# Performance work log

Hardware: AMD Instinct MI355X
Metric: run time of the kernel (lower is better)

The kernel has to match this reference:

```python
import jax, jax.numpy as jnp
import numpy as np

B, T, D = 32, 1024, 768
H = 768          # GRU hidden size
INNER = 512      # fc output size
NOUT = 39        # out_proj outputs (13 classes x 3 ACCDOA coords)


def setup_inputs() -> dict:
    key = jax.random.key(0)
    ks = jax.random.split(key, 16)
    s_in = 1.0 / np.sqrt(H)
    inp = {
        "features": jax.random.normal(ks[0], (B, T, D), jnp.float32),
        "padding_mask": jnp.zeros((B, T), jnp.bool_),
        # GRU layer 0 (input D -> H), PyTorch gate order [r, z, n]
        "w_ih0": jax.random.uniform(ks[1], (3 * H, D), jnp.float32, -s_in, s_in),
        "w_hh0": jax.random.uniform(ks[2], (3 * H, H), jnp.float32, -s_in, s_in),
        "b_ih0": jax.random.uniform(ks[3], (3 * H,), jnp.float32, -s_in, s_in),
        "b_hh0": jax.random.uniform(ks[4], (3 * H,), jnp.float32, -s_in, s_in),
        # GRU layer 1 (H -> H)
        "w_ih1": jax.random.uniform(ks[5], (3 * H, H), jnp.float32, -s_in, s_in),
        "w_hh1": jax.random.uniform(ks[6], (3 * H, H), jnp.float32, -s_in, s_in),
        "b_ih1": jax.random.uniform(ks[7], (3 * H,), jnp.float32, -s_in, s_in),
        "b_hh1": jax.random.uniform(ks[8], (3 * H,), jnp.float32, -s_in, s_in),
        # fc: hidden -> inner, then SELU
        "fc_w": jax.random.uniform(ks[9], (INNER, H), jnp.float32, -s_in, s_in),
        "fc_b": jax.random.uniform(ks[10], (INNER,), jnp.float32, -s_in, s_in),
        # out_proj: inner -> num_outs, then tanh
        "out_w": jax.random.uniform(ks[11], (NOUT, INNER), jnp.float32, -1.0 / np.sqrt(INNER), 1.0 / np.sqrt(INNER)),
        "out_b": jax.random.uniform(ks[12], (NOUT,), jnp.float32, -1.0 / np.sqrt(INNER), 1.0 / np.sqrt(INNER)),
    }
    return inp


def _gru_layer(x, w_ih, w_hh, b_ih, b_hh):
    # x: [B, T, Din] -> [B, T, H]; PyTorch GRU math, gate order r,z,n
    b, t, _ = x.shape
    h = w_hh.shape[1]
    # precompute input projections for all timesteps in one big GEMM
    x_proj = jnp.einsum('btd,gd->btg', x, w_ih) + b_ih  # [B, T, 3H]

    def step(h_prev, xp):
        gi_r, gi_z, gi_n = jnp.split(xp, 3, axis=-1)
        gh = h_prev @ w_hh.T + b_hh
        gh_r, gh_z, gh_n = jnp.split(gh, 3, axis=-1)
        r = jax.nn.sigmoid(gi_r + gh_r)
        z = jax.nn.sigmoid(gi_z + gh_z)
        n = jnp.tanh(gi_n + r * gh_n)
        h_new = (1.0 - z) * n + z * h_prev
        return h_new, h_new

    h0 = jnp.zeros((b, h), x.dtype)
    _, ys = jax.lax.scan(step, h0, jnp.swapaxes(x_proj, 0, 1))  # ys: [T, B, H]
    return jnp.swapaxes(ys, 0, 1)


def reference(features, padding_mask, w_ih0, w_hh0, b_ih0, b_hh0,
              w_ih1, w_hh1, b_ih1, b_hh1, fc_w, fc_b, out_w, out_b):
    # dropout_input p=0.0 -> identity (eval); padding_mask unused by forward math
    x = _gru_layer(features, w_ih0, w_hh0, b_ih0, b_hh0)
    x = _gru_layer(x, w_ih1, w_hh1, b_ih1, b_hh1)
    x = jax.nn.selu(x @ fc_w.T + fc_b)          # fc + activation_fn='selu'
    x = jnp.tanh(x @ out_w.T + out_b)           # out_proj + out_activation 'tanh'
    return x
```

## Files before the change

kernel.cpp:

```cpp
#include <hip/hip_runtime.h>
#include <cstdint>

#define GB_M 128
#define GB_N 64
#define GB_K 16

__global__ __launch_bounds__(256) void gemm_bt_f32(
    const float* __restrict__ A, const float* __restrict__ B,
    const float* __restrict__ bias, float* __restrict__ C,
    int Mc, int N, int K, int tc_shift, int Tfull, int t0, int act)
{
  __shared__ float As[GB_K][GB_M + 4];
  __shared__ float Bs[GB_K][GB_N + 4];
  const int tid = threadIdx.x;
  const int m0 = blockIdx.y * GB_M;
  const int n0 = blockIdx.x * GB_N;
  const int tx = tid & 15;
  const int ty = tid >> 4;

  const int tcmask = (1 << tc_shift) - 1;
  int arow[2];
#pragma unroll
  for (int i = 0; i < 2; i++) {
    int f = tid + i * 256;
    int row = f >> 2;
    int rc = m0 + row;
    arow[i] = (rc >> tc_shift) * Tfull + t0 + (rc & tcmask);
  }
  const int akq = tid & 3;
  const int brow = tid >> 2;
  const int bn = n0 + brow;

  float acc[8][4];
#pragma unroll
  for (int i = 0; i < 8; i++)
#pragma unroll
    for (int j = 0; j < 4; j++) acc[i][j] = 0.f;

  for (int k0 = 0; k0 < K; k0 += GB_K) {
#pragma unroll
    for (int i = 0; i < 2; i++) {
      int f = tid + i * 256;
      int row = f >> 2;
      float4 v = *(const float4*)(A + (size_t)arow[i] * K + k0 + akq * 4);
      As[akq * 4 + 0][row] = v.x; As[akq * 4 + 1][row] = v.y;
      As[akq * 4 + 2][row] = v.z; As[akq * 4 + 3][row] = v.w;
    }
    {
      float4 v = make_float4(0.f, 0.f, 0.f, 0.f);
      if (bn < N) v = *(const float4*)(B + (size_t)bn * K + k0 + akq * 4);
      Bs[akq * 4 + 0][brow] = v.x; Bs[akq * 4 + 1][brow] = v.y;
      Bs[akq * 4 + 2][brow] = v.z; Bs[akq * 4 + 3][brow] = v.w;
    }
    __syncthreads();
#pragma unroll
    for (int k = 0; k < GB_K; k++) {
      float4 a0 = *(const float4*)&As[k][ty * 8];
      float4 a1 = *(const float4*)&As[k][ty * 8 + 4];
      float4 b0 = *(const float4*)&Bs[k][tx * 4];
      float av[8] = {a0.x, a0.y, a0.z, a0.w, a1.x, a1.y, a1.z, a1.w};
      float bv[4] = {b0.x, b0.y, b0.z, b0.w};
#pragma unroll
      for (int i = 0; i < 8; i++)
#pragma unroll
        for (int j = 0; j < 4; j++) acc[i][j] += av[i] * bv[j];
    }
    __syncthreads();
  }

#pragma unroll
  for (int j = 0; j < 4; j++) {
    int n = n0 + tx * 4 + j;
    if (n >= N) continue;
    float bz = bias[n];
#pragma unroll
    for (int i = 0; i < 8; i++) {
      int m = m0 + ty * 8 + i;
      float x = acc[i][j] + bz;
      if (act == 1) {
        x = 1.0507009873554805f * (x > 0.f ? x : 1.6732632423543772f * (__expf(x) - 1.f));
      } else if (act == 2) {
        x = tanhf(x);
      }
      C[(size_t)m * N + n] = x;
    }
  }
}

#define RT 384
#define RNWG 256

__device__ __forceinline__ void pollge(const unsigned* fp, unsigned want) {
  while (__hip_atomic_load(fp, __ATOMIC_RELAXED, __HIP_MEMORY_SCOPE_AGENT) < want)
    __builtin_amdgcn_s_sleep(1);
}

__global__ __launch_bounds__(RT, 1) void gru_rec(
    const float* __restrict__ gi, const float* __restrict__ w_hh,
    const float* __restrict__ b_hh, float* __restrict__ hb,
    unsigned* __restrict__ flags, float* __restrict__ seq,
    int t0, int Tc)
{
  __shared__ float Wl[36][776];
  __shared__ float hs[8][776];
  const int wg = blockIdx.x;
  const int jg = wg & 63;
  const int sd = wg >> 6;
  const int j0 = jg * 12;
  const int tid = threadIdx.x;
  const int p  = tid >> 6;
  const int ks = tid & 63;

  unsigned* flagX_my = flags + (((0 * 4 + sd) * 64) + jg) * 16;
  unsigned* flagY_my = flags + (((1 * 4 + sd) * 64) + jg) * 16;

  for (int f = tid; f < 36 * 192; f += RT) {
    int row = f / 192;
    int kq = f - row * 192;
    int gate = row / 12;
    int jl = row - gate * 12;
    float4 v = *(const float4*)(w_hh + (size_t)(gate * 768 + j0 + jl) * 768 + kq * 4);
    *(float4*)&Wl[row][kq * 4] = v;
  }

  const int j2l = (ks >> 2) & 1;
  const int cl  = ks & 3;
  const int j_out  = j0 + 2 * p + j2l;
  const int bX_out = 8 * sd + cl;
  const int bY_out = 8 * sd + 4 + cl;
  const float bhr = b_hh[j_out];
  const float bhz = b_hh[768 + j_out];
  const float bhn = b_hh[1536 + j_out];

  const float* wb[3][2];
#pragma unroll
  for (int g = 0; g < 3; g++)
#pragma unroll
    for (int j2 = 0; j2 < 2; j2++)
      wb[g][j2] = &Wl[g * 12 + 2 * p + j2][0];

  const int sbi = tid / 96;
  const int sk  = tid - sbi * 96;
  const int jgA = (sk * 8) / 12;
  const int jgB = (sk * 8 + 7) / 12;
  const unsigned* fXA = flags + ((0 * 4 + sd) * 64 + jgA) * 16;
  const unsigned* fXB = flags + ((0 * 4 + sd) * 64 + jgB) * 16;
  const unsigned* fYA = flags + ((1 * 4 + sd) * 64 + jgA) * 16;
  const unsigned* fYB = flags + ((1 * 4 + sd) * 64 + jgB) * 16;

  const bool hi4 = (ks & 4) != 0;
  const bool hi2 = (ks & 2) != 0;
  const bool hi1 = (ks & 1) != 0;

  for (int tt = 0; tt < Tc; tt++) {
    const int t = t0 + tt;

    pollge(fXA, (unsigned)t);
    pollge(fXB, (unsigned)t);
    {
      const unsigned long long* src = (const unsigned long long*)
          (hb + (size_t)(t & 1) * 24576 + (size_t)(8 * sd + sbi) * 768) + sk * 4;
      unsigned long long v[4];
#pragma unroll
      for (int i = 0; i < 4; i++)
        v[i] = __hip_atomic_load(src + i, __ATOMIC_RELAXED, __HIP_MEMORY_SCOPE_AGENT);
      float* dst = &hs[sbi][sk * 8];
      *(float4*)dst = make_float4(
          __uint_as_float((unsigned)v[0]), __uint_as_float((unsigned)(v[0] >> 32)),
          __uint_as_float((unsigned)v[1]), __uint_as_float((unsigned)(v[1] >> 32)));
      *(float4*)(dst + 4) = make_float4(
          __uint_as_float((unsigned)v[2]), __uint_as_float((unsigned)(v[2] >> 32)),
          __uint_as_float((unsigned)v[3]), __uint_as_float((unsigned)(v[3] >> 32)));
    }
    float gXr = 0.f, gXz = 0.f, gXn = 0.f;
    if (ks < 8) {
      const float* gX = gi + ((size_t)bX_out * Tc + tt) * 2304 + j_out;
      gXr = gX[0]; gXz = gX[768]; gXn = gX[1536];
    }
    __syncthreads();
    if (tid == 0)
      __hip_atomic_store(flagY_my, (unsigned)t, __ATOMIC_RELAXED, __HIP_MEMORY_SCOPE_AGENT);

    float r3[3];
    {
      float acc[3][2][4];
#pragma unroll
      for (int g = 0; g < 3; g++)
#pragma unroll
        for (int j2 = 0; j2 < 2; j2++)
#pragma unroll
          for (int c = 0; c < 4; c++) acc[g][j2][c] = 0.f;
#pragma unroll
      for (int kk = 0; kk < 3; kk++) {
        const int off = (kk * 64 + ks) * 4;
        float4 h[4];
#pragma unroll
        for (int c = 0; c < 4; c++) h[c] = *(const float4*)(&hs[c][0] + off);
#pragma unroll
        for (int g = 0; g < 3; g++)
#pragma unroll
          for (int j2 = 0; j2 < 2; j2++) {
            float4 w = *(const float4*)(wb[g][j2] + off);
#pragma unroll
            for (int c = 0; c < 4; c++)
              acc[g][j2][c] += w.x * h[c].x + w.y * h[c].y + w.z * h[c].z + w.w * h[c].w;
          }
      }
      float r12[3][4];
#pragma unroll
      for (int g = 0; g < 3; g++)
#pragma unroll
        for (int c = 0; c < 4; c++) {
          float send = hi4 ? acc[g][0][c] : acc[g][1][c];
          float keep = hi4 ? acc[g][1][c] : acc[g][0][c];
          r12[g][c] = keep + __shfl_xor(send, 4);
        }
      float r6[3][2];
#pragma unroll
      for (int g = 0; g < 3; g++)
#pragma unroll
        for (int c2 = 0; c2 < 2; c2++) {
          float send = hi2 ? r12[g][c2] : r12[g][2 + c2];
          float keep = hi2 ? r12[g][2 + c2] : r12[g][c2];
          r6[g][c2] = keep + __shfl_xor(send, 2);
        }
#pragma unroll
      for (int g = 0; g < 3; g++) {
        float send = hi1 ? r6[g][0] : r6[g][1];
        float keep = hi1 ? r6[g][1] : r6[g][0];
        r3[g] = keep + __shfl_xor(send, 1);
      }
#pragma unroll
      for (int g = 0; g < 3; g++) {
        r3[g] += __shfl_xor(r3[g], 8);
        r3[g] += __shfl_xor(r3[g], 16);
        r3[g] += __shfl_xor(r3[g], 32);
      }
    }
    if (ks < 8) {
      float hp = hs[cl][j_out];
      float r = 1.f / (1.f + __expf(-(gXr + r3[0] + bhr)));
      float z = 1.f / (1.f + __expf(-(gXz + r3[1] + bhz)));
      float n = tanhf(gXn + r * (r3[2] + bhn));
      float hv = (1.f - z) * n + z * hp;
      __hip_atomic_store(hb + (size_t)((t + 1) & 1) * 24576 + (size_t)bX_out * 768 + j_out,
                         hv, __ATOMIC_RELAXED, __HIP_MEMORY_SCOPE_AGENT);
      seq[((size_t)bX_out * 1024 + t) * 768 + j_out] = hv;
    }

    pollge(fYA, (unsigned)t);
    pollge(fYB, (unsigned)t);
    {
      const unsigned long long* src = (const unsigned long long*)
          (hb + (size_t)(t & 1) * 24576 + (size_t)(8 * sd + 4 + sbi) * 768) + sk * 4;
      unsigned long long v[4];
#pragma unroll
      for (int i = 0; i < 4; i++)
        v[i] = __hip_atomic_load(src + i, __ATOMIC_RELAXED, __HIP_MEMORY_SCOPE_AGENT);
      float* dst = &hs[4 + sbi][sk * 8];
      *(float4*)dst = make_float4(
          __uint_as_float((unsigned)v[0]), __uint_as_float((unsigned)(v[0] >> 32)),
          __uint_as_float((unsigned)v[1]), __uint_as_float((unsigned)(v[1] >> 32)));
      *(float4*)(dst + 4) = make_float4(
          __uint_as_float((unsigned)v[2]), __uint_as_float((unsigned)(v[2] >> 32)),
          __uint_as_float((unsigned)v[3]), __uint_as_float((unsigned)(v[3] >> 32)));
    }
    float gYr = 0.f, gYz = 0.f, gYn = 0.f;
    if (ks < 8) {
      const float* gY = gi + ((size_t)bY_out * Tc + tt) * 2304 + j_out;
      gYr = gY[0]; gYz = gY[768]; gYn = gY[1536];
    }
    __syncthreads();
    if (tid == 0)
      __hip_atomic_store(flagX_my, (unsigned)(t + 1), __ATOMIC_RELAXED, __HIP_MEMORY_SCOPE_AGENT);

    {
      float acc[3][2][4];
#pragma unroll
      for (int g = 0; g < 3; g++)
#pragma unroll
        for (int j2 = 0; j2 < 2; j2++)
#pragma unroll
          for (int c = 0; c < 4; c++) acc[g][j2][c] = 0.f;
#pragma unroll
      for (int kk = 0; kk < 3; kk++) {
        const int off = (kk * 64 + ks) * 4;
        float4 h[4];
#pragma unroll
        for (int c = 0; c < 4; c++) h[c] = *(const float4*)(&hs[4 + c][0] + off);
#pragma unroll
        for (int g = 0; g < 3; g++)
#pragma unroll
          for (int j2 = 0; j2 < 2; j2++) {
            float4 w = *(const float4*)(wb[g][j2] + off);
#pragma unroll
            for (int c = 0; c < 4; c++)
              acc[g][j2][c] += w.x * h[c].x + w.y * h[c].y + w.z * h[c].z + w.w * h[c].w;
          }
      }
      float r12[3][4];
#pragma unroll
      for (int g = 0; g < 3; g++)
#pragma unroll
        for (int c = 0; c < 4; c++) {
          float send = hi4 ? acc[g][0][c] : acc[g][1][c];
          float keep = hi4 ? acc[g][1][c] : acc[g][0][c];
          r12[g][c] = keep + __shfl_xor(send, 4);
        }
      float r6[3][2];
#pragma unroll
      for (int g = 0; g < 3; g++)
#pragma unroll
        for (int c2 = 0; c2 < 2; c2++) {
          float send = hi2 ? r12[g][c2] : r12[g][2 + c2];
          float keep = hi2 ? r12[g][2 + c2] : r12[g][c2];
          r6[g][c2] = keep + __shfl_xor(send, 2);
        }
#pragma unroll
      for (int g = 0; g < 3; g++) {
        float send = hi1 ? r6[g][0] : r6[g][1];
        float keep = hi1 ? r6[g][1] : r6[g][0];
        r3[g] = keep + __shfl_xor(send, 1);
      }
#pragma unroll
      for (int g = 0; g < 3; g++) {
        r3[g] += __shfl_xor(r3[g], 8);
        r3[g] += __shfl_xor(r3[g], 16);
        r3[g] += __shfl_xor(r3[g], 32);
      }
    }
    if (ks < 8) {
      float hp = hs[4 + cl][j_out];
      float r = 1.f / (1.f + __expf(-(gYr + r3[0] + bhr)));
      float z = 1.f / (1.f + __expf(-(gYz + r3[1] + bhz)));
      float n = tanhf(gYn + r * (r3[2] + bhn));
      float hv = (1.f - z) * n + z * hp;
      __hip_atomic_store(hb + (size_t)((t + 1) & 1) * 24576 + (size_t)bY_out * 768 + j_out,
                         hv, __ATOMIC_RELAXED, __HIP_MEMORY_SCOPE_AGENT);
      seq[((size_t)bY_out * 1024 + t) * 768 + j_out] = hv;
    }
  }
  __syncthreads();
  if (tid == 0)
    __hip_atomic_store(flagY_my, (unsigned)(t0 + Tc), __ATOMIC_RELAXED, __HIP_MEMORY_SCOPE_AGENT);
}

extern "C" void kernel_launch(void* const* d_in, const int* in_sizes, int n_in,
                              void* d_out, int out_size, void* d_ws, size_t ws_size,
                              hipStream_t stream) {
  const float* feat  = (const float*)d_in[0];
  const float* w_ih0 = (const float*)d_in[2];
  const float* w_hh0 = (const float*)d_in[3];
  const float* b_ih0 = (const float*)d_in[4];
  const float* b_hh0 = (const float*)d_in[5];
  const float* w_ih1 = (const float*)d_in[6];
  const float* w_hh1 = (const float*)d_in[7];
  const float* b_ih1 = (const float*)d_in[8];
  const float* b_hh1 = (const float*)d_in[9];
  const float* fc_w  = (const float*)d_in[10];
  const float* fc_b  = (const float*)d_in[11];
  const float* out_w = (const float*)d_in[12];
  const float* out_b = (const float*)d_in[13];
  float* out = (float*)d_out;

  const int Tc = 256;
  const int McChunk = 32 * Tc;

  float* proj = (float*)d_ws;
  float* seq  = proj + (size_t)32 * Tc * 2304;
  float* hbuf = seq + (size_t)25165824;
  unsigned* flags = (unsigned*)(hbuf + 2 * 24576);

  hipMemsetAsync(hbuf, 0, 2 * 24576 * sizeof(float), stream);
  hipMemsetAsync(flags, 0, 32768, stream);
  for (int c = 0; c < 4; c++) {
    gemm_bt_f32<<<dim3(36, McChunk / 128), dim3(256), 0, stream>>>(
        feat, w_ih0, b_ih0, proj, McChunk, 2304, 768, 8, 1024, c * Tc, 0);
    gru_rec<<<dim3(RNWG), dim3(RT), 0, stream>>>(
        proj, w_hh0, b_hh0, hbuf, flags, seq, c * Tc, Tc);
  }
  hipMemsetAsync(hbuf, 0, 2 * 24576 * sizeof(float), stream);
  hipMemsetAsync(flags, 0, 32768, stream);
  for (int c = 0; c < 4; c++) {
    gemm_bt_f32<<<dim3(36, McChunk / 128), dim3(256), 0, stream>>>(
        seq, w_ih1, b_ih1, proj, McChunk, 2304, 768, 8, 1024, c * Tc, 0);
    gru_rec<<<dim3(RNWG), dim3(RT), 0, stream>>>(
        proj, w_hh1, b_hh1, hbuf, flags, seq, c * Tc, Tc);
  }
  gemm_bt_f32<<<dim3(8, 256), dim3(256), 0, stream>>>(
      seq, fc_w, fc_b, proj, 32768, 512, 768, 15, 32768, 0, 1);
  gemm_bt_f32<<<dim3(1, 256), dim3(256), 0, stream>>>(
      proj, out_w, out_b, out, 32768, 39, 512, 15, 32768, 0, 2);
}
```

Measured before the change: 15.27 ms.

## Keep GRU recurrent weights in registers and use packed FMA math

Each thread now loads its slice of the recurrent weight matrix into 18 float4 registers once, instead of staging all weights in shared memory and re-reading them every timestep. The dot products are rewritten as packed two-wide FMAs on vf2 vectors, with the two lanes summed at the end. A 64KB dynamic LDS allocation is added to the launch, likely to keep one workgroup per CU so the persistent flag-synchronised kernel is not co-scheduled. Register pressure rises substantially (72 extra VGPRs for weights), which could cause spills at 384 threads.

```diff
diff --git a/kernel.cpp b/kernel.cpp
--- a/kernel.cpp
+++ b/kernel.cpp
@@ -1,5 +1,7 @@
 #include <hip/hip_runtime.h>
 #include <cstdint>
+
+typedef float vf2 __attribute__((ext_vector_type(2)));
 
 #define GB_M 128
 #define GB_N 64
@@ -101,7 +103,6 @@
     unsigned* __restrict__ flags, float* __restrict__ seq,
     int t0, int Tc)
 {
-  __shared__ float Wl[36][776];
   __shared__ float hs[8][776];
   const int wg = blockIdx.x;
   const int jg = wg & 63;
@@ -114,14 +115,15 @@
   unsigned* flagX_my = flags + (((0 * 4 + sd) * 64) + jg) * 16;
   unsigned* flagY_my = flags + (((1 * 4 + sd) * 64) + jg) * 16;
 
-  for (int f = tid; f < 36 * 192; f += RT) {
-    int row = f / 192;
-    int kq = f - row * 192;
-    int gate = row / 12;
-    int jl = row - gate * 12;
-    float4 v = *(const float4*)(w_hh + (size_t)(gate * 768 + j0 + jl) * 768 + kq * 4);
-    *(float4*)&Wl[row][kq * 4] = v;
-  }
+  float4 wreg[3][2][3];
+#pragma unroll
+  for (int g = 0; g < 3; g++)
+#pragma unroll
+    for (int j2 = 0; j2 < 2; j2++)
+#pragma unroll
+      for (int kk = 0; kk < 3; kk++)
+        wreg[g][j2][kk] = *(const float4*)(
+            w_hh + (size_t)(g * 768 + j0 + 2 * p + j2) * 768 + (kk * 64 + ks) * 4);
 
   const int j2l = (ks >> 2) & 1;
   const int cl  = ks & 3;
@@ -131,13 +133,6 @@
   const float bhr = b_hh[j_out];
   const float bhz = b_hh[768 + j_out];
   const float bhn = b_hh[1536 + j_out];
-
-  const float* wb[3][2];
-#pragma unroll
-  for (int g = 0; g < 3; g++)
-#pragma unroll
-    for (int j2 = 0; j2 < 2; j2++)
-      wb[g][j2] = &Wl[g * 12 + 2 * p + j2][0];
 
   const int sbi = tid / 96;
   const int sk  = tid - sbi * 96;
@@ -183,29 +178,45 @@
 
     float r3[3];
     {
-      float acc[3][2][4];
+      vf2 a2[3][2][4];
 #pragma unroll
       for (int g = 0; g < 3; g++)
 #pragma unroll
         for (int j2 = 0; j2 < 2; j2++)
 #pragma unroll
-          for (int c = 0; c < 4; c++) acc[g][j2][c] = 0.f;
+          for (int c = 0; c < 4; c++) a2[g][j2][c] = (vf2)(0.f);
 #pragma unroll
       for (int kk = 0; kk < 3; kk++) {
         const int off = (kk * 64 + ks) * 4;
-        float4 h[4];
-#pragma unroll
-        for (int c = 0; c < 4; c++) h[c] = *(const float4*)(&hs[c][0] + off);
+        vf2 hlo[4], hhi[4];
+#pragma unroll
+        for (int c = 0; c < 4; c++) {
+          float4 h = *(const float4*)(&hs[c][0] + off);
+          hlo[c] = (vf2){h.x, h.y};
+          hhi[c] = (vf2){h.z, h.w};
+        }
 #pragma unroll
         for (int g = 0; g < 3; g++)
 #pragma unroll
           for (int j2 = 0; j2 < 2; j2++) {
-            float4 w = *(const float4*)(wb[g][j2] + off);
-#pragma unroll
-            for (int c = 0; c < 4; c++)
-              acc[g][j2][c] += w.x * h[c].x + w.y * h[c].y + w.z * h[c].z + w.w * h[c].w;
+            float4 w = wreg[g][j2][kk];
+            vf2 wlo = (vf2){w.x, w.y};
+            vf2 whi = (vf2){w.z, w.w};
+#pragma unroll
+            for (int c = 0; c < 4; c++) {
+              a2[g][j2][c] = __builtin_elementwise_fma(wlo, hlo[c], a2[g][j2][c]);
+              a2[g][j2][c] = __builtin_elementwise_fma(whi, hhi[c], a2[g][j2][c]);
+            }
           }
       }
+      float acc[3][2][4];
+#pragma unroll
+      for (int g = 0; g < 3; g++)
+#pragma unroll
+        for (int j2 = 0; j2 < 2; j2++)
+#pragma unroll
+          for (int c = 0; c < 4; c++) acc[g][j2][c] = a2[g][j2][c].x + a2[g][j2][c].y;
+
       float r12[3][4];
 #pragma unroll
       for (int g = 0; g < 3; g++)
@@ -275,29 +286,45 @@
       __hip_atomic_store(flagX_my, (unsigned)(t + 1), __ATOMIC_RELAXED, __HIP_MEMORY_SCOPE_AGENT);
 
     {
-      float acc[3][2][4];
+      vf2 a2[3][2][4];
 #pragma unroll
       for (int g = 0; g < 3; g++)
 #pragma unroll
         for (int j2 = 0; j2 < 2; j2++)
 #pragma unroll
-          for (int c = 0; c < 4; c++) acc[g][j2][c] = 0.f;
+          for (int c = 0; c < 4; c++) a2[g][j2][c] = (vf2)(0.f);
 #pragma unroll
       for (int kk = 0; kk < 3; kk++) {
         const int off = (kk * 64 + ks) * 4;
-        float4 h[4];
-#pragma unroll
-        for (int c = 0; c < 4; c++) h[c] = *(const float4*)(&hs[4 + c][0] + off);
+        vf2 hlo[4], hhi[4];
+#pragma unroll
+        for (int c = 0; c < 4; c++) {
+          float4 h = *(const float4*)(&hs[4 + c][0] + off);
+          hlo[c] = (vf2){h.x, h.y};
+          hhi[c] = (vf2){h.z, h.w};
+        }
 #pragma unroll
         for (int g = 0; g < 3; g++)
 #pragma unroll
           for (int j2 = 0; j2 < 2; j2++) {
-            float4 w = *(const float4*)(wb[g][j2] + off);
-#pragma unroll
-            for (int c = 0; c < 4; c++)
-              acc[g][j2][c] += w.x * h[c].x + w.y * h[c].y + w.z * h[c].z + w.w * h[c].w;
+            float4 w = wreg[g][j2][kk];
+            vf2 wlo = (vf2){w.x, w.y};
+            vf2 whi = (vf2){w.z, w.w};
+#pragma unroll
+            for (int c = 0; c < 4; c++) {
+              a2[g][j2][c] = __builtin_elementwise_fma(wlo, hlo[c], a2[g][j2][c]);
+              a2[g][j2][c] = __builtin_elementwise_fma(whi, hhi[c], a2[g][j2][c]);
+            }
           }
       }
+      float acc[3][2][4];
+#pragma unroll
+      for (int g = 0; g < 3; g++)
+#pragma unroll
+        for (int j2 = 0; j2 < 2; j2++)
+#pragma unroll
+          for (int c = 0; c < 4; c++) acc[g][j2][c] = a2[g][j2][c].x + a2[g][j2][c].y;
+
       float r12[3][4];
 #pragma unroll
       for (int g = 0; g < 3; g++)
@@ -365,6 +392,7 @@
 
   const int Tc = 256;
   const int McChunk = 32 * Tc;
+  const size_t DYN_LDS = 65536;
 
   float* proj = (float*)d_ws;
   float* seq  = proj + (size_t)32 * Tc * 2304;
@@ -376,7 +404,7 @@
   for (int c = 0; c < 4; c++) {
     gemm_bt_f32<<<dim3(36, McChunk / 128), dim3(256), 0, stream>>>(
         feat, w_ih0, b_ih0, proj, McChunk, 2304, 768, 8, 1024, c * Tc, 0);
-    gru_rec<<<dim3(RNWG), dim3(RT), 0, stream>>>(
+    gru_rec<<<dim3(RNWG), dim3(RT), DYN_LDS, stream>>>(
         proj, w_hh0, b_hh0, hbuf, flags, seq, c * Tc, Tc);
   }
   hipMemsetAsync(hbuf, 0, 2 * 24576 * sizeof(float), stream);
@@ -384,7 +412,7 @@
   for (int c = 0; c < 4; c++) {
     gemm_bt_f32<<<dim3(36, McChunk / 128), dim3(256), 0, stream>>>(
         seq, w_ih1, b_ih1, proj, McChunk, 2304, 768, 8, 1024, c * Tc, 0);
-    gru_rec<<<dim3(RNWG), dim3(RT), 0, stream>>>(
+    gru_rec<<<dim3(RNWG), dim3(RT), DYN_LDS, stream>>>(
         proj, w_hh1, b_hh1, hbuf, flags, seq, c * Tc, Tc);
   }
   gemm_bt_f32<<<dim3(8, 256), dim3(256), 0, stream>>>(
```

Result: faster. 14.06 ms (-7.9%).
